# Optimization experiments

Hardware: AMD Instinct MI355X
Metric: run time of the kernel (lower is better)

Reference implementation:

```python
import jax, jax.numpy as jnp
import numpy as np
import math

DIM = 1024
HEAD = 16


def setup_inputs() -> dict:
    key = jax.random.key(0)
    k1, k2, k3, k4, k5 = jax.random.split(key, 5)
    scale = 1.0 / math.sqrt(DIM)
    return {
        "x": jax.random.normal(k1, (2, 2048, DIM), dtype=jnp.float32),
        "W_kqv": jax.random.uniform(k2, (3 * DIM, DIM), minval=-scale, maxval=scale, dtype=jnp.float32),
        "b_kqv": jax.random.uniform(k3, (3 * DIM,), minval=-scale, maxval=scale, dtype=jnp.float32),
        "W_out": jax.random.uniform(k4, (DIM, DIM), minval=-scale, maxval=scale, dtype=jnp.float32),
        "b_out": jax.random.uniform(k5, (DIM,), minval=-scale, maxval=scale, dtype=jnp.float32),
    }


def reference(x, W_kqv, b_kqv, W_out, b_out):
    b, s, h = x.shape
    head = HEAD
    d = h // head
    # fused QKV projection (torch Linear: x @ W.T + b)
    kqv = jnp.einsum("bsh,oh->bso", x, W_kqv) + b_kqv  # [b, s, 3h]
    q, k, v = jnp.split(kqv, 3, axis=-1)
    # [b, s, h] -> [b, head, s, d]
    q = q.reshape(b, s, head, d).transpose(0, 2, 1, 3)
    k = k.reshape(b, s, head, d).transpose(0, 2, 1, 3)
    v = v.reshape(b, s, head, d).transpose(0, 2, 1, 3)
    scores = jnp.einsum("bnqd,bnkd->bnqk", q, k) / jnp.sqrt(jnp.float32(d))
    attn = jax.nn.softmax(scores, axis=-1)
    ctx = jnp.einsum("bnqk,bnkd->bnqd", attn, v)  # [b, head, s, d]
    ctx = ctx.transpose(0, 2, 1, 3).reshape(b, s, h)
    return jnp.einsum("bsh,oh->bso", ctx, W_out) + b_out
```

## Files before the change

kernel.cpp:

```cpp
#include <hip/hip_runtime.h>
#include <hip/hip_bf16.h>

#define DIM   1024
#define NHEAD 16
#define HD    64
#define SEQ   2048
#define BATCH 2
#define QKV3  3072

using short8 = __attribute__((ext_vector_type(8))) short;
using f32x4  = __attribute__((ext_vector_type(4))) float;

__device__ inline short f2bf(float f) {
    union { float f; unsigned u; } x; x.f = f;
    const unsigned r = (x.u + 0x7FFFu + ((x.u >> 16) & 1u)) >> 16;
    return (short)r;
}
__device__ inline unsigned pkbf(float a, float b) {
    union { __hip_bfloat162 h; unsigned u; } cv;
    cv.h = __float22bfloat162_rn(make_float2(a, b));
    return cv.u;
}

__device__ __forceinline__ void g2l16(const void* gptr, void* ldsbase) {
    __builtin_amdgcn_global_load_lds(
        (const __attribute__((address_space(1))) unsigned int*)(unsigned long long)gptr,
        (__attribute__((address_space(3))) unsigned int*)(unsigned int)(unsigned long long)ldsbase,
        16, 0, 0);
}

__global__ __launch_bounds__(256)
void conv_bf16(const float* __restrict__ x, const float* __restrict__ wk,
               const float* __restrict__ wo,
               unsigned short* __restrict__ xb, unsigned short* __restrict__ wkb,
               unsigned short* __restrict__ wob)
{
    const int bid = blockIdx.x;
    const float* src; unsigned short* dst; size_t base;
    if (bid < 1024)      { src = x;  dst = xb;  base = (size_t)bid * 4096; }
    else if (bid < 1792) { src = wk; dst = wkb; base = (size_t)(bid - 1024) * 4096; }
    else                 { src = wo; dst = wob; base = (size_t)(bid - 1792) * 4096; }
    const size_t off = base + threadIdx.x * 16;
    const float4 f0 = *(const float4*)(src + off + 0);
    const float4 f1 = *(const float4*)(src + off + 4);
    const float4 f2 = *(const float4*)(src + off + 8);
    const float4 f3 = *(const float4*)(src + off + 12);
    uint4 o0, o1;
    o0.x = pkbf(f0.x, f0.y); o0.y = pkbf(f0.z, f0.w);
    o0.z = pkbf(f1.x, f1.y); o0.w = pkbf(f1.z, f1.w);
    o1.x = pkbf(f2.x, f2.y); o1.y = pkbf(f2.z, f2.w);
    o1.z = pkbf(f3.x, f3.y); o1.w = pkbf(f3.z, f3.w);
    *(uint4*)(dst + off + 0) = o0;
    *(uint4*)(dst + off + 8) = o1;
}

__global__ __launch_bounds__(256)
void gemm_qkv(const unsigned short* __restrict__ A, const unsigned short* __restrict__ B,
              const float* __restrict__ bias,
              unsigned short* __restrict__ qbf, unsigned short* __restrict__ kbf,
              unsigned short* __restrict__ vtbf)
{
    constexpr int BK = 32, NIT = DIM / BK;
    const int K = DIM;
    __shared__ short As[2][128 * BK];
    __shared__ short Bs[2][128 * BK];

    const int tid  = threadIdx.x;
    const int lane = tid & 63;
    const int wave = tid >> 6;
    const int quad = lane >> 4;
    const int ln   = lane & 15;
    const int wm   = (wave & 1) * 64;
    const int wn   = (wave >> 1) * 64;

    const int bid = blockIdx.x;
    const int xcd = bid & 7;
    const int t   = bid >> 3;
    const int m0  = (xcd * 4 + (t & 3)) * 128;
    const int n0  = (t >> 2) * 128;

    int srow[2], sg[2];
#pragma unroll
    for (int i = 0; i < 2; ++i) {
        const int c  = wave * 128 + i * 64 + lane;
        srow[i] = c >> 2;
        sg[i]   = (c & 3) ^ ((srow[i] >> 1) & 3);
    }

    f32x4 acc[4][4];
#pragma unroll
    for (int i = 0; i < 4; ++i)
#pragma unroll
        for (int j = 0; j < 4; ++j) acc[i][j] = (f32x4){0.f, 0.f, 0.f, 0.f};

#pragma unroll
    for (int i = 0; i < 2; ++i) {
        const int cb = wave * 128 + i * 64;
        g2l16(A + (size_t)(m0 + srow[i]) * K + sg[i] * 8, &As[0][cb * 8]);
        g2l16(B + (size_t)(n0 + srow[i]) * K + sg[i] * 8, &Bs[0][cb * 8]);
    }
    __syncthreads();

    for (int kt = 0; kt < NIT; ++kt) {
        const int p = kt & 1;
        if (kt + 1 < NIT) {
            const int kn = (kt + 1) * BK;
#pragma unroll
            for (int i = 0; i < 2; ++i) {
                const int cb = wave * 128 + i * 64;
                g2l16(A + (size_t)(m0 + srow[i]) * K + kn + sg[i] * 8, &As[1 - p][cb * 8]);
                g2l16(B + (size_t)(n0 + srow[i]) * K + kn + sg[i] * 8, &Bs[1 - p][cb * 8]);
            }
        }

        short8 a[4], b[4];
#pragma unroll
        for (int i = 0; i < 4; ++i) {
            const int row = wm + i * 16 + ln;
            const int ch  = quad ^ ((row >> 1) & 3);
            a[i] = *(const short8*)&As[p][row * BK + ch * 8];
        }
#pragma unroll
        for (int j = 0; j < 4; ++j) {
            const int row = wn + j * 16 + ln;
            const int ch  = quad ^ ((row >> 1) & 3);
            b[j] = *(const short8*)&Bs[p][row * BK + ch * 8];
        }
#pragma unroll
        for (int i = 0; i < 4; ++i)
#pragma unroll
            for (int j = 0; j < 4; ++j)
                acc[i][j] = __builtin_amdgcn_mfma_f32_16x16x32_bf16(
                    a[i], b[j], acc[i][j], 0, 0, 0);
        __syncthreads();
    }

#pragma unroll
    for (int j = 0; j < 4; ++j) {
        const int col = n0 + wn + j * 16 + ln;
        const int sel = col >> 10;
        const int c   = col & 1023;
        const int hh  = c >> 6;
        const int dd  = c & 63;
        const float bv = bias[col];
        if (sel < 2) {
            unsigned short* dst = (sel == 0) ? qbf : kbf;
            const float qs = (sel == 0) ? 0.18033688f : 1.0f;
#pragma unroll
            for (int i = 0; i < 4; ++i)
#pragma unroll
                for (int r2 = 0; r2 < 4; ++r2) {
                    const int row = m0 + wm + i * 16 + quad * 4 + r2;
                    const int bb = row >> 11, ss = row & 2047;
                    dst[((size_t)(bb * NHEAD + hh) * SEQ + ss) * HD + dd] =
                        (unsigned short)f2bf((acc[i][j][r2] + bv) * qs);
                }
        } else {
            const int row0 = m0 + wm + quad * 4;
            const int bb = row0 >> 11;
            const size_t vbase = ((size_t)(bb * NHEAD + hh) * HD + dd) * SEQ;
#pragma unroll
            for (int i = 0; i < 4; ++i) {
                const int ss0 = (row0 & 2047) + i * 16;
                uint2 pk;
                pk.x = pkbf(acc[i][j][0] + bv, acc[i][j][1] + bv);
                pk.y = pkbf(acc[i][j][2] + bv, acc[i][j][3] + bv);
                *(uint2*)&vtbf[vbase + ss0] = pk;
            }
        }
    }
}

__global__ __launch_bounds__(256)
void attn_flash_mfma(const unsigned short* __restrict__ qbf,
                     const unsigned short* __restrict__ kbf,
                     const unsigned short* __restrict__ vtbf,
                     unsigned short* __restrict__ ctxbf)
{
    __shared__ short Ks[2][64 * 64];
    __shared__ short Vt[2][64 * 64];

    const int tid  = threadIdx.x;
    const int lane = tid & 63;
    const int wave = tid >> 6;
    const int quad = lane >> 4;
    const int ln   = lane & 15;

    const int bid = blockIdx.x;
    const int bh  = bid & 31;
    const int qt  = bid >> 5;
    const int q0  = qt * 128;
    const int b   = bh >> 4;
    const int h   = bh & 15;

    const size_t sbase = (size_t)bh * SEQ * HD;
    const size_t vbase = (size_t)bh * HD * SEQ;

    int srw[2], scg[2];
#pragma unroll
    for (int it = 0; it < 2; ++it) {
        const int ch = tid + it * 256;
        srw[it] = ch >> 3;
        scg[it] = (ch & 7) ^ (srw[it] & 7);
    }

    short8 qf[2][2];
#pragma unroll
    for (int sm = 0; sm < 2; ++sm)
#pragma unroll
        for (int kc = 0; kc < 2; ++kc)
            qf[sm][kc] = *(const short8*)&qbf[sbase +
                (size_t)(q0 + wave * 32 + sm * 16 + ln) * HD + kc * 32 + quad * 8];

#pragma unroll
    for (int it = 0; it < 2; ++it) {
        const int cb = tid + it * 256;
        g2l16(kbf + sbase + (size_t)srw[it] * HD + scg[it] * 8, &Ks[0][cb * 8]);
        g2l16(vtbf + vbase + (size_t)srw[it] * SEQ + scg[it] * 8, &Vt[0][cb * 8]);
    }
    __syncthreads();

    f32x4 O[2][4];
#pragma unroll
    for (int sm = 0; sm < 2; ++sm)
#pragma unroll
        for (int dj = 0; dj < 4; ++dj) O[sm][dj] = (f32x4){0.f, 0.f, 0.f, 0.f};
    f32x4 lacc[2];
    lacc[0] = (f32x4){0.f, 0.f, 0.f, 0.f};
    lacc[1] = (f32x4){0.f, 0.f, 0.f, 0.f};

    short8 vone;
#pragma unroll
    for (int t = 0; t < 8; ++t) vone[t] = (short)0x3F80;

    for (int kt = 0; kt < SEQ / 64; ++kt) {
        const int p = kt & 1;
        if (kt + 1 < SEQ / 64) {
            const int k0n = (kt + 1) * 64;
#pragma unroll
            for (int it = 0; it < 2; ++it) {
                const int cb = tid + it * 256;
                g2l16(kbf + sbase + (size_t)(k0n + srw[it]) * HD + scg[it] * 8,
                      &Ks[1 - p][cb * 8]);
                g2l16(vtbf + vbase + (size_t)srw[it] * SEQ + k0n + scg[it] * 8,
                      &Vt[1 - p][cb * 8]);
            }
        }

        f32x4 st[2][4];
#pragma unroll
        for (int j = 0; j < 4; ++j) {
            const int row = j * 16 + ln;
            const int c0 = quad ^ (row & 7);
            const int c1 = (4 + quad) ^ (row & 7);
            const short8 kf0 = *(const short8*)&Ks[p][row * 64 + c0 * 8];
            const short8 kf1 = *(const short8*)&Ks[p][row * 64 + c1 * 8];
#pragma unroll
            for (int sm = 0; sm < 2; ++sm) {
                f32x4 tt = __builtin_amdgcn_mfma_f32_16x16x32_bf16(
                    kf0, qf[sm][0], (f32x4){0.f, 0.f, 0.f, 0.f}, 0, 0, 0);
                st[sm][j] = __builtin_amdgcn_mfma_f32_16x16x32_bf16(
                    kf1, qf[sm][1], tt, 0, 0, 0);
            }
        }

        short8 pf[2][2];
#pragma unroll
        for (int sm = 0; sm < 2; ++sm) {
            unsigned lo[4], hi[4];
#pragma unroll
            for (int j = 0; j < 4; ++j) {
                const float e0 = __builtin_amdgcn_exp2f(st[sm][j][0]);
                const float e1 = __builtin_amdgcn_exp2f(st[sm][j][1]);
                const float e2 = __builtin_amdgcn_exp2f(st[sm][j][2]);
                const float e3 = __builtin_amdgcn_exp2f(st[sm][j][3]);
                lo[j] = pkbf(e0, e1);
                hi[j] = pkbf(e2, e3);
            }
#pragma unroll
            for (int kc = 0; kc < 2; ++kc) {
                auto sa = __builtin_amdgcn_permlane32_swap(lo[2 * kc], lo[2 * kc + 1], false, false);
                auto sb = __builtin_amdgcn_permlane32_swap(hi[2 * kc], hi[2 * kc + 1], false, false);
                auto ua = __builtin_amdgcn_permlane16_swap(sa[0], sa[1], false, false);
                auto ub = __builtin_amdgcn_permlane16_swap(sb[0], sb[1], false, false);
                union { unsigned u[4]; short8 s; } cv;
                cv.u[0] = ua[0];
                cv.u[1] = ub[0];
                cv.u[2] = ua[1];
                cv.u[3] = ub[1];
                pf[sm][kc] = cv.s;
            }
        }

#pragma unroll
        for (int kc = 0; kc < 2; ++kc) {
            lacc[0] = __builtin_amdgcn_mfma_f32_16x16x32_bf16(pf[0][kc], vone, lacc[0], 0, 0, 0);
            lacc[1] = __builtin_amdgcn_mfma_f32_16x16x32_bf16(pf[1][kc], vone, lacc[1], 0, 0, 0);
#pragma unroll
            for (int dj = 0; dj < 4; ++dj) {
                const int row = dj * 16 + ln;
                const int cg  = (kc * 4 + quad) ^ (row & 7);
                const short8 vf = *(const short8*)&Vt[p][row * 64 + cg * 8];
                O[0][dj] = __builtin_amdgcn_mfma_f32_16x16x32_bf16(pf[0][kc], vf, O[0][dj], 0, 0, 0);
                O[1][dj] = __builtin_amdgcn_mfma_f32_16x16x32_bf16(pf[1][kc], vf, O[1][dj], 0, 0, 0);
            }
        }
        __syncthreads();
    }

#pragma unroll
    for (int sm = 0; sm < 2; ++sm)
#pragma unroll
        for (int r2 = 0; r2 < 4; ++r2) {
            const float inv = 1.0f / lacc[sm][r2];
            const int row = b * SEQ + q0 + wave * 32 + sm * 16 + quad * 4 + r2;
#pragma unroll
            for (int dj = 0; dj < 4; ++dj)
                ctxbf[(size_t)row * DIM + h * HD + dj * 16 + ln] =
                    (unsigned short)f2bf(O[sm][dj][r2] * inv);
        }
}

__global__ __launch_bounds__(256)
void gemm_out(const unsigned short* __restrict__ A, const unsigned short* __restrict__ B,
              const float* __restrict__ bias, float* __restrict__ C)
{
    constexpr int BK = 32, NIT = DIM / BK;
    const int K = DIM, N = DIM;
    __shared__ short As[2][128 * BK];
    __shared__ short Bs[2][64 * BK];

    const int tid  = threadIdx.x;
    const int lane = tid & 63;
    const int wave = tid >> 6;
    const int quad = lane >> 4;
    const int ln   = lane & 15;
    const int wm   = (wave & 1) * 64;
    const int wn   = (wave >> 1) * 32;

    const int bid = blockIdx.x;
    const int xcd = bid & 7;
    const int t   = bid >> 3;
    const int m0  = (xcd * 4 + (t & 3)) * 128;
    const int n0  = (t >> 2) * 64;

    int srow[2], sg[2];
#pragma unroll
    for (int i = 0; i < 2; ++i) {
        const int c  = wave * 128 + i * 64 + lane;
        srow[i] = c >> 2;
        sg[i]   = (c & 3) ^ ((srow[i] >> 1) & 3);
    }
    const int cB  = wave * 64 + lane;
    const int brow = cB >> 2;
    const int bg   = (cB & 3) ^ ((brow >> 1) & 3);

    f32x4 acc[4][2];
#pragma unroll
    for (int i = 0; i < 4; ++i)
#pragma unroll
        for (int j = 0; j < 2; ++j) acc[i][j] = (f32x4){0.f, 0.f, 0.f, 0.f};

#pragma unroll
    for (int i = 0; i < 2; ++i)
        g2l16(A + (size_t)(m0 + srow[i]) * K + sg[i] * 8,
              &As[0][(wave * 128 + i * 64) * 8]);
    g2l16(B + (size_t)(n0 + brow) * K + bg * 8, &Bs[0][(wave * 64) * 8]);
    __syncthreads();

    for (int kt = 0; kt < NIT; ++kt) {
        const int p = kt & 1;
        if (kt + 1 < NIT) {
            const int kn = (kt + 1) * BK;
#pragma unroll
            for (int i = 0; i < 2; ++i)
                g2l16(A + (size_t)(m0 + srow[i]) * K + kn + sg[i] * 8,
                      &As[1 - p][(wave * 128 + i * 64) * 8]);
            g2l16(B + (size_t)(n0 + brow) * K + kn + bg * 8, &Bs[1 - p][(wave * 64) * 8]);
        }

        short8 a[4], b[2];
#pragma unroll
        for (int i = 0; i < 4; ++i) {
            const int row = wm + i * 16 + ln;
            const int ch  = quad ^ ((row >> 1) & 3);
            a[i] = *(const short8*)&As[p][row * BK + ch * 8];
        }
#pragma unroll
        for (int j = 0; j < 2; ++j) {
            const int row = wn + j * 16 + ln;
            const int ch  = quad ^ ((row >> 1) & 3);
            b[j] = *(const short8*)&Bs[p][row * BK + ch * 8];
        }
#pragma unroll
        for (int i = 0; i < 4; ++i)
#pragma unroll
            for (int j = 0; j < 2; ++j)
                acc[i][j] = __builtin_amdgcn_mfma_f32_16x16x32_bf16(
                    a[i], b[j], acc[i][j], 0, 0, 0);
        __syncthreads();
    }

#pragma unroll
    for (int j = 0; j < 2; ++j) {
        const int col = n0 + wn + j * 16 + ln;
        const float bv = bias[col];
#pragma unroll
        for (int i = 0; i < 4; ++i)
#pragma unroll
            for (int r2 = 0; r2 < 4; ++r2) {
                const int row = m0 + wm + i * 16 + quad * 4 + r2;
                C[(size_t)row * N + col] = acc[i][j][r2] + bv;
            }
    }
}

extern "C" void kernel_launch(void* const* d_in, const int* in_sizes, int n_in,
                              void* d_out, int out_size, void* d_ws, size_t ws_size,
                              hipStream_t stream)
{
    const float* x     = (const float*)d_in[0];
    const float* W_kqv = (const float*)d_in[1];
    const float* b_kqv = (const float*)d_in[2];
    const float* W_out = (const float*)d_in[3];
    const float* b_out = (const float*)d_in[4];
    float* out = (float*)d_out;

    char* w = (char*)d_ws;
    unsigned short* qbf   = (unsigned short*)w;  w += (size_t)BATCH * NHEAD * SEQ * HD * 2;
    unsigned short* kbf   = (unsigned short*)w;  w += (size_t)BATCH * NHEAD * SEQ * HD * 2;
    unsigned short* vtbf  = (unsigned short*)w;  w += (size_t)BATCH * NHEAD * HD * SEQ * 2;
    unsigned short* ctxbf = (unsigned short*)w;  w += (size_t)BATCH * SEQ * DIM * 2;
    unsigned short* xb    = (unsigned short*)w;  w += (size_t)BATCH * SEQ * DIM * 2;
    unsigned short* wkb   = (unsigned short*)w;  w += (size_t)QKV3 * DIM * 2;
    unsigned short* wob   = (unsigned short*)w;

    dim3 blk(256);

    conv_bf16<<<dim3(2048), blk, 0, stream>>>(x, W_kqv, W_out, xb, wkb, wob);

    gemm_qkv<<<dim3(768), blk, 0, stream>>>(xb, wkb, b_kqv, qbf, kbf, vtbf);

    attn_flash_mfma<<<dim3(512), blk, 0, stream>>>(qbf, kbf, vtbf, ctxbf);

    gemm_out<<<dim3(512), blk, 0, stream>>>(ctxbf, wob, b_out, out);
}
```

Measured before the change: 186.1 us.

## Split KV range across two wave groups per attention block and merge via LDS

The attention block grows to 512 threads. Each group of four waves handles half of the key/value sequence for the same 128 query rows, with its own double-buffered K/V tiles in LDS. After the loop, the first half writes its partial O and row sums into LDS, and the second half adds them, normalizes and stores the context. This halves the serial key loop per wave and raises waves per CU. The cost is doubled LDS per block and an extra LDS merge step. s_setprio hints are also added around the MFMA sections.

```diff
diff --git a/kernel.cpp b/kernel.cpp
--- a/kernel.cpp
+++ b/kernel.cpp
@@ -171,18 +171,20 @@
     }
 }
 
-__global__ __launch_bounds__(256)
+__global__ __launch_bounds__(512)
 void attn_flash_mfma(const unsigned short* __restrict__ qbf,
                      const unsigned short* __restrict__ kbf,
                      const unsigned short* __restrict__ vtbf,
                      unsigned short* __restrict__ ctxbf)
 {
-    __shared__ short Ks[2][64 * 64];
-    __shared__ short Vt[2][64 * 64];
+    __shared__ short Ks[2][2][64 * 64];
+    __shared__ short Vt[2][2][64 * 64];
 
     const int tid  = threadIdx.x;
     const int lane = tid & 63;
     const int wave = tid >> 6;
+    const int hf   = wave >> 2;
+    const int w4   = wave & 3;
     const int quad = lane >> 4;
     const int ln   = lane & 15;
 
@@ -195,11 +197,13 @@
 
     const size_t sbase = (size_t)bh * SEQ * HD;
     const size_t vbase = (size_t)bh * HD * SEQ;
-
+    const int kv0 = hf * (SEQ / 2);
+
+    const int tloc = tid & 255;
     int srw[2], scg[2];
 #pragma unroll
     for (int it = 0; it < 2; ++it) {
-        const int ch = tid + it * 256;
+        const int ch = tloc + it * 256;
         srw[it] = ch >> 3;
         scg[it] = (ch & 7) ^ (srw[it] & 7);
     }
@@ -210,13 +214,15 @@
 #pragma unroll
         for (int kc = 0; kc < 2; ++kc)
             qf[sm][kc] = *(const short8*)&qbf[sbase +
-                (size_t)(q0 + wave * 32 + sm * 16 + ln) * HD + kc * 32 + quad * 8];
+                (size_t)(q0 + w4 * 32 + sm * 16 + ln) * HD + kc * 32 + quad * 8];
 
 #pragma unroll
     for (int it = 0; it < 2; ++it) {
-        const int cb = tid + it * 256;
-        g2l16(kbf + sbase + (size_t)srw[it] * HD + scg[it] * 8, &Ks[0][cb * 8]);
-        g2l16(vtbf + vbase + (size_t)srw[it] * SEQ + scg[it] * 8, &Vt[0][cb * 8]);
+        const int cb = tloc + it * 256;
+        g2l16(kbf + sbase + (size_t)(kv0 + srw[it]) * HD + scg[it] * 8,
+              &Ks[0][hf][cb * 8]);
+        g2l16(vtbf + vbase + (size_t)srw[it] * SEQ + kv0 + scg[it] * 8,
+              &Vt[0][hf][cb * 8]);
     }
     __syncthreads();
 
@@ -233,28 +239,30 @@
 #pragma unroll
     for (int t = 0; t < 8; ++t) vone[t] = (short)0x3F80;
 
-    for (int kt = 0; kt < SEQ / 64; ++kt) {
+    constexpr int NIT = (SEQ / 2) / 64;
+    for (int kt = 0; kt < NIT; ++kt) {
         const int p = kt & 1;
-        if (kt + 1 < SEQ / 64) {
-            const int k0n = (kt + 1) * 64;
+        if (kt + 1 < NIT) {
+            const int k0n = kv0 + (kt + 1) * 64;
 #pragma unroll
             for (int it = 0; it < 2; ++it) {
-                const int cb = tid + it * 256;
+                const int cb = tloc + it * 256;
                 g2l16(kbf + sbase + (size_t)(k0n + srw[it]) * HD + scg[it] * 8,
-                      &Ks[1 - p][cb * 8]);
+                      &Ks[1 - p][hf][cb * 8]);
                 g2l16(vtbf + vbase + (size_t)srw[it] * SEQ + k0n + scg[it] * 8,
-                      &Vt[1 - p][cb * 8]);
+                      &Vt[1 - p][hf][cb * 8]);
             }
         }
 
         f32x4 st[2][4];
+        __builtin_amdgcn_s_setprio(1);
 #pragma unroll
         for (int j = 0; j < 4; ++j) {
             const int row = j * 16 + ln;
             const int c0 = quad ^ (row & 7);
             const int c1 = (4 + quad) ^ (row & 7);
-            const short8 kf0 = *(const short8*)&Ks[p][row * 64 + c0 * 8];
-            const short8 kf1 = *(const short8*)&Ks[p][row * 64 + c1 * 8];
+            const short8 kf0 = *(const short8*)&Ks[p][hf][row * 64 + c0 * 8];
+            const short8 kf1 = *(const short8*)&Ks[p][hf][row * 64 + c1 * 8];
 #pragma unroll
             for (int sm = 0; sm < 2; ++sm) {
                 f32x4 tt = __builtin_amdgcn_mfma_f32_16x16x32_bf16(
@@ -263,6 +271,7 @@
                     kf1, qf[sm][1], tt, 0, 0, 0);
             }
         }
+        __builtin_amdgcn_s_setprio(0);
 
         short8 pf[2][2];
 #pragma unroll
@@ -292,6 +301,7 @@
             }
         }
 
+        __builtin_amdgcn_s_setprio(1);
 #pragma unroll
         for (int kc = 0; kc < 2; ++kc) {
             lacc[0] = __builtin_amdgcn_mfma_f32_16x16x32_bf16(pf[0][kc], vone, lacc[0], 0, 0, 0);
@@ -300,25 +310,49 @@
             for (int dj = 0; dj < 4; ++dj) {
                 const int row = dj * 16 + ln;
                 const int cg  = (kc * 4 + quad) ^ (row & 7);
-                const short8 vf = *(const short8*)&Vt[p][row * 64 + cg * 8];
+                const short8 vf = *(const short8*)&Vt[p][hf][row * 64 + cg * 8];
                 O[0][dj] = __builtin_amdgcn_mfma_f32_16x16x32_bf16(pf[0][kc], vf, O[0][dj], 0, 0, 0);
                 O[1][dj] = __builtin_amdgcn_mfma_f32_16x16x32_bf16(pf[1][kc], vf, O[1][dj], 0, 0, 0);
             }
         }
+        __builtin_amdgcn_s_setprio(0);
         __syncthreads();
     }
 
-#pragma unroll
-    for (int sm = 0; sm < 2; ++sm)
-#pragma unroll
-        for (int r2 = 0; r2 < 4; ++r2) {
-            const float inv = 1.0f / lacc[sm][r2];
-            const int row = b * SEQ + q0 + wave * 32 + sm * 16 + quad * 4 + r2;
+    float* Of = (float*)&Ks[0][0][0];
+    float* Lf = (float*)&Vt[0][0][0];
+    if (hf == 0) {
+#pragma unroll
+        for (int sm = 0; sm < 2; ++sm) {
 #pragma unroll
             for (int dj = 0; dj < 4; ++dj)
-                ctxbf[(size_t)row * DIM + h * HD + dj * 16 + ln] =
-                    (unsigned short)f2bf(O[sm][dj][r2] * inv);
-        }
+#pragma unroll
+                for (int r2 = 0; r2 < 4; ++r2)
+                    Of[(w4 * 32 + sm * 16 + quad * 4 + r2) * 64 + dj * 16 + ln] =
+                        O[sm][dj][r2];
+            if (ln == 0)
+#pragma unroll
+                for (int r2 = 0; r2 < 4; ++r2)
+                    Lf[w4 * 32 + sm * 16 + quad * 4 + r2] = lacc[sm][r2];
+        }
+    }
+    __syncthreads();
+    if (hf == 1) {
+#pragma unroll
+        for (int sm = 0; sm < 2; ++sm)
+#pragma unroll
+            for (int r2 = 0; r2 < 4; ++r2) {
+                const int rr = w4 * 32 + sm * 16 + quad * 4 + r2;
+                const float inv = 1.0f / (lacc[sm][r2] + Lf[rr]);
+                const int row = b * SEQ + q0 + rr;
+#pragma unroll
+                for (int dj = 0; dj < 4; ++dj) {
+                    const float val = O[sm][dj][r2] + Of[rr * 64 + dj * 16 + ln];
+                    ctxbf[(size_t)row * DIM + h * HD + dj * 16 + ln] =
+                        (unsigned short)f2bf(val * inv);
+                }
+            }
+    }
 }
 
 __global__ __launch_bounds__(256)
@@ -441,7 +475,7 @@
 
     gemm_qkv<<<dim3(768), blk, 0, stream>>>(xb, wkb, b_kqv, qbf, kbf, vtbf);
 
-    attn_flash_mfma<<<dim3(512), blk, 0, stream>>>(qbf, kbf, vtbf, ctxbf);
+    attn_flash_mfma<<<dim3(512), dim3(512), 0, stream>>>(qbf, kbf, vtbf, ctxbf);
 
     gemm_out<<<dim3(512), blk, 0, stream>>>(ctxbf, wob, b_out, out);
 }
```

Result: faster. 175.9 us (-5.5%).
